# Kernel optimization log

Hardware: AMD Instinct MI355X
Metric: run time of the kernel (lower is better)

Reference implementation:

```python
import jax, jax.numpy as jnp
import numpy as np

B, T, D = 4096, 200, 64
N_USERS, N_ITEMS = 100000, 100000


def _linear_init(k, out_dim, in_dim):
    kw, kb = jax.random.split(k)
    lim = 1.0 / np.sqrt(in_dim)
    w = jax.random.uniform(kw, (out_dim, in_dim), minval=-lim, maxval=lim, dtype=jnp.float32)
    b = jax.random.uniform(kb, (out_dim,), minval=-lim, maxval=lim, dtype=jnp.float32)
    return w, b


def setup_inputs() -> dict:
    key = jax.random.key(0)
    ks = jax.random.split(key, 16)
    gru_w_ih, gru_b_ih = _linear_init(ks[0], 3 * D, D)   # torch GRU gate order: r, z, n
    gru_w_hh, gru_b_hh = _linear_init(ks[1], 3 * D, D)
    attn_w, attn_b = _linear_init(ks[2], D, D)
    wr_w, wr_b = _linear_init(ks[3], D, 2 * D)
    wz_w, wz_b = _linear_init(ks[4], D, 2 * D)
    wh_w, wh_b = _linear_init(ks[5], D, 2 * D)
    aux_w, aux_b = _linear_init(ks[6], 1, D)
    item_emb = jax.random.normal(ks[7], (N_ITEMS + 1, D), dtype=jnp.float32)
    user_bias = jax.random.normal(ks[8], (N_USERS, 1), dtype=jnp.float32) * 0.01
    item_bias = jax.random.normal(ks[9], (N_ITEMS, 1), dtype=jnp.float32) * 0.01
    u_idx = jax.random.randint(ks[10], (B,), 0, N_USERS)
    i_idx = jax.random.randint(ks[11], (B,), 0, N_ITEMS)
    seq = jax.random.randint(ks[12], (B, T), 0, N_ITEMS + 1)
    return dict(u_idx=u_idx, i_idx=i_idx, seq=seq,
                item_emb=item_emb, user_bias=user_bias, item_bias=item_bias,
                gru_w_ih=gru_w_ih, gru_b_ih=gru_b_ih, gru_w_hh=gru_w_hh, gru_b_hh=gru_b_hh,
                attn_w=attn_w, attn_b=attn_b,
                wr_w=wr_w, wr_b=wr_b, wz_w=wz_w, wz_b=wz_b, wh_w=wh_w, wh_b=wh_b,
                aux_w=aux_w, aux_b=aux_b)


def _gru(seq_emb, w_ih, b_ih, w_hh, b_hh):
    # seq_emb: [B, T, D]. Precompute input projections for all timesteps.
    x_proj = jnp.einsum('btd,gd->btg', seq_emb, w_ih) + b_ih  # [B, T, 3D]
    x_proj = jnp.transpose(x_proj, (1, 0, 2))                 # [T, B, 3D]
    h0 = jnp.zeros((seq_emb.shape[0], D), dtype=seq_emb.dtype)

    def step(h, xp):
        gh = h @ w_hh.T + b_hh
        xr, xz, xn = jnp.split(xp, 3, axis=-1)
        hr, hz, hn = jnp.split(gh, 3, axis=-1)
        r = jax.nn.sigmoid(xr + hr)
        z = jax.nn.sigmoid(xz + hz)
        n = jnp.tanh(xn + r * hn)
        h_new = (1.0 - z) * n + z * h
        return h_new, h_new

    _, hs = jax.lax.scan(step, h0, x_proj)
    return jnp.transpose(hs, (1, 0, 2))  # [B, T, D]


def _augru(seq_emb, attn_w_t, wr_w, wr_b, wz_w, wz_b, wh_w, wh_b):
    # Split each [D, 2D] weight into x-part and h-part (input was concat([x, h])).
    wr_x, wr_h = wr_w[:, :D], wr_w[:, D:]
    wz_x, wz_h = wz_w[:, :D], wz_w[:, D:]
    wh_x, wh_h = wh_w[:, :D], wh_w[:, D:]
    xr = jnp.einsum('btd,hd->bth', seq_emb, wr_x) + wr_b  # [B, T, D]
    xz = jnp.einsum('btd,hd->bth', seq_emb, wz_x) + wz_b
    xh = jnp.einsum('btd,hd->bth', seq_emb, wh_x) + wh_b
    h0 = jnp.zeros((seq_emb.shape[0], D), dtype=seq_emb.dtype)
    inputs = (jnp.transpose(xr, (1, 0, 2)), jnp.transpose(xz, (1, 0, 2)),
              jnp.transpose(xh, (1, 0, 2)), attn_w_t.T)  # [T,B,D]x3, [T,B]

    def step(h, inp):
        xr_t, xz_t, xh_t, a_t = inp
        r = jax.nn.sigmoid(xr_t + h @ wr_h.T)
        z = jax.nn.sigmoid(xz_t + h @ wz_h.T)
        h_hat = jnp.tanh(xh_t + (r * h) @ wh_h.T)
        z = a_t[:, None] * z
        h_new = (1.0 - z) * h + z * h_hat
        return h_new, None

    h_final, _ = jax.lax.scan(step, h0, inputs)
    return h_final  # [B, D]


def reference(u_idx, i_idx, seq, item_emb, user_bias, item_bias,
              gru_w_ih, gru_b_ih, gru_w_hh, gru_b_hh, attn_w, attn_b,
              wr_w, wr_b, wz_w, wz_b, wh_w, wh_b, aux_w, aux_b):
    fm1 = user_bias[u_idx] + item_bias[i_idx]          # [B, 1]
    target_emb = item_emb[i_idx]                       # [B, D]
    seq_emb = item_emb[seq]                            # [B, T, D]

    gru_out = _gru(seq_emb, gru_w_ih, gru_b_ih, gru_w_hh, gru_b_hh)  # [B, T, D]

    target_proj = target_emb @ attn_w.T + attn_b       # [B, D]
    attn_scores = jnp.einsum('btd,bd->bt', gru_out, target_proj)
    attn_weights = jax.nn.sigmoid(attn_scores)         # [B, T]

    attn_vec = _augru(seq_emb, attn_weights, wr_w, wr_b, wz_w, wz_b, wh_w, wh_b)  # [B, D]

    aux_logits = (gru_out[:, -1, :] @ aux_w.T + aux_b)[:, 0]  # [B]
    return (fm1, attn_vec, aux_logits)
```

## Files before the change

### kernel.cpp

```cpp
#include <hip/hip_runtime.h>

typedef __bf16 bf16x8 __attribute__((ext_vector_type(8)));
typedef float f32x4 __attribute__((ext_vector_type(4)));

#define T_LEN 200
#define NB 4096

__device__ __forceinline__ f32x4 mfma16(bf16x8 a, bf16x8 b, f32x4 c) {
    return __builtin_amdgcn_mfma_f32_16x16x32_bf16(a, b, c, 0, 0, 0);
}
__device__ __forceinline__ float sigf(float x) {
    return __builtin_amdgcn_rcpf(1.0f + __expf(-x));
}
__device__ __forceinline__ float tanh_fast(float x) {
    return 1.0f - 2.0f * __builtin_amdgcn_rcpf(__expf(2.0f * x) + 1.0f);
}

__device__ __forceinline__ unsigned packRNE2(float a, float b) {
    unsigned ha = (unsigned)__builtin_bit_cast(unsigned short, (__bf16)a);
    unsigned hb = (unsigned)__builtin_bit_cast(unsigned short, (__bf16)b);
    return ha | (hb << 16);
}
__device__ __forceinline__ void publish_hi(unsigned short* hp, float v) {
    __bf16 h = (__bf16)v;
    *hp = __builtin_bit_cast(unsigned short, h);
}

struct Frag { bf16x8 hi, lo; };
__device__ __forceinline__ Frag make_frag(f32x4 a, f32x4 b) {
    Frag f;
    #pragma unroll
    for (int j = 0; j < 4; j++) {
        float v = a[j]; __bf16 h = (__bf16)v;
        f.hi[j] = h; f.lo[j] = (__bf16)(v - (float)h);
    }
    #pragma unroll
    for (int j = 0; j < 4; j++) {
        float v = b[j]; __bf16 h = (__bf16)v;
        f.hi[4 + j] = h; f.lo[4 + j] = (__bf16)(v - (float)h);
    }
    return f;
}
__device__ __forceinline__ bf16x8 load_w(const float* p) {
    f32x4 a = *(const f32x4*)p, b = *(const f32x4*)(p + 4);
    bf16x8 w;
    #pragma unroll
    for (int j = 0; j < 4; j++) { w[j] = (__bf16)a[j]; w[4 + j] = (__bf16)b[j]; }
    return w;
}

__global__ __launch_bounds__(512, 2)
void dien_fused(const int* __restrict__ u_idx, const int* __restrict__ i_idx,
                const int* __restrict__ seq, const float* __restrict__ item_emb,
                const float* __restrict__ user_bias, const float* __restrict__ item_bias,
                const float* __restrict__ gw_ih, const float* __restrict__ gb_ih,
                const float* __restrict__ gw_hh, const float* __restrict__ gb_hh,
                const float* __restrict__ attn_w, const float* __restrict__ attn_b,
                const float* __restrict__ wr_w, const float* __restrict__ wr_b,
                const float* __restrict__ wz_w, const float* __restrict__ wz_b,
                const float* __restrict__ wh_w, const float* __restrict__ wh_b,
                const float* __restrict__ aux_w, const float* __restrict__ aux_b,
                float* __restrict__ out)
{
    __shared__ int sSeq[16][T_LEN];
    __shared__ __align__(16) float sTP[16][64];
    __shared__ __align__(16) unsigned short sHGhi[16][72];
    __shared__ __align__(16) unsigned short sHAhi[16][72];
    __shared__ __align__(16) unsigned short sRHhi[16][72];
    __shared__ __align__(16) unsigned short sXhi[16][72];
    __shared__ float sScore[2][16];
    __shared__ float sParts[16][4];

    const int tid  = threadIdx.x;
    const int wave = tid >> 6;
    const int lane = tid & 63;
    const int c    = lane & 15;
    const int q    = lane >> 4;
    const bool isG = (wave < 4);
    const int wg   = wave & 3;
    const int dglob = wg * 16 + c;
    const int row0 = blockIdx.x * 16;

    for (int i = tid; i < 16 * T_LEN; i += 512) {
        int b = i / T_LEN, t = i - b * T_LEN;
        sSeq[b][t] = seq[(row0 + b) * T_LEN + t];
    }

    if (tid < 16) {
        int b = row0 + tid;
        out[b] = user_bias[u_idx[b]] + item_bias[i_idx[b]];
    }

    if (tid < 256) {
        int b  = tid >> 4;
        int d0 = (tid & 15) * 4;
        const float* erow = item_emb + (long)i_idx[row0 + b] * 64;
        float e[64];
        #pragma unroll
        for (int k4 = 0; k4 < 16; k4++) {
            f32x4 v = *(const f32x4*)(erow + k4 * 4);
            #pragma unroll
            for (int j = 0; j < 4; j++) e[k4 * 4 + j] = v[j];
        }
        #pragma unroll
        for (int dd = 0; dd < 4; dd++) {
            int d = d0 + dd;
            const float* wrow = attn_w + d * 64;
            float s = attn_b[d];
            #pragma unroll
            for (int k4 = 0; k4 < 16; k4++) {
                f32x4 wv = *(const f32x4*)(wrow + k4 * 4);
                #pragma unroll
                for (int j = 0; j < 4; j++) s += e[k4 * 4 + j] * wv[j];
            }
            sTP[b][d] = s;
        }
    }

    for (int i = tid; i < 16 * 72; i += 512) sHAhi[0][i] = 0;
    const int xrow = wg * 4 + (lane >> 4);
    const int xch  = lane & 15;
    if (isG) {
        const float* p = item_emb + (long)seq[(row0 + xrow) * T_LEN + 0] * 64 + xch * 4;
        f32x4 v = *(const f32x4*)p;
        *(uint2*)&sXhi[xrow][xch * 4] =
            make_uint2(packRNE2(v[0], v[1]), packRNE2(v[2], v[3]));
    }
    __syncthreads();

    bf16x8 W[12];
    if (isG) {
        #pragma unroll
        for (int g = 0; g < 3; g++)
            #pragma unroll
            for (int s = 0; s < 2; s++) {
                W[g * 2 + s]     = load_w(gw_ih + (g * 64 + dglob) * 64 + s * 32 + q * 8);
                W[6 + g * 2 + s] = load_w(gw_hh + (g * 64 + dglob) * 64 + s * 32 + q * 8);
            }
    } else {
        #pragma unroll
        for (int s = 0; s < 2; s++) {
            const int fo = dglob * 128 + s * 32 + q * 8;
            W[0 + s]  = load_w(wr_w + fo);
            W[2 + s]  = load_w(wr_w + fo + 64);
            W[4 + s]  = load_w(wz_w + fo);
            W[6 + s]  = load_w(wz_w + fo + 64);
            W[8 + s]  = load_w(wh_w + fo);
            W[10 + s] = load_w(wh_w + fo + 64);
        }
    }

    float bA, bB, bC, bD;
    if (isG) {
        bA = gb_ih[dglob] + gb_hh[dglob];
        bB = gb_ih[64 + dglob] + gb_hh[64 + dglob];
        bC = gb_ih[128 + dglob];
        bD = gb_hh[128 + dglob];
    } else {
        bA = wr_b[dglob];
        bB = wz_b[dglob];
        bC = wh_b[dglob];
        bD = 0.0f;
    }
    const float auxwc = aux_w[dglob];

    Frag tpB0, tpB1;
    if (isG) {
        tpB0 = make_frag(*(const f32x4*)&sTP[c][q * 8], *(const f32x4*)&sTP[c][q * 8 + 4]);
        tpB1 = make_frag(*(const f32x4*)&sTP[c][32 + q * 8], *(const f32x4*)&sTP[c][32 + q * 8 + 4]);
    }

    float hst[4] = {0.f, 0.f, 0.f, 0.f};
    bf16x8 fr0, fr1;
    #pragma unroll
    for (int j = 0; j < 8; j++) { fr0[j] = (__bf16)0.f; fr1[j] = (__bf16)0.f; }
    f32x4 aAH = {0.f, 0.f, 0.f, 0.f};
    float z_c[4] = {0.f, 0.f, 0.f, 0.f};

    f32x4 xnxt = {0.f, 0.f, 0.f, 0.f};
    if (isG) {
        int t1 = (T_LEN > 1) ? 1 : 0;
        xnxt = *(const f32x4*)(item_emb + (long)sSeq[xrow][t1] * 64 + xch * 4);
    }

    for (int t = 0; t < T_LEN; t++) {
        f32x4 xg;
        f32x4 aAR, aAZ;

        bf16x8 x0 = *(const bf16x8*)&sXhi[c][q * 8];
        bf16x8 x1 = *(const bf16x8*)&sXhi[c][32 + q * 8];

        if (isG) {
            int tn = t + 2; if (tn > T_LEN - 1) tn = T_LEN - 1;
            xg = *(const f32x4*)(item_emb + (long)sSeq[xrow][tn] * 64 + xch * 4);

            f32x4 accR = {bA, bA, bA, bA};
            accR = mfma16(x0, W[0], accR); accR = mfma16(x1, W[1], accR);
            accR = mfma16(fr0, W[6], accR); accR = mfma16(fr1, W[7], accR);
            f32x4 accZ = {bB, bB, bB, bB};
            accZ = mfma16(x0, W[2], accZ); accZ = mfma16(x1, W[3], accZ);
            accZ = mfma16(fr0, W[8], accZ); accZ = mfma16(fr1, W[9], accZ);
            f32x4 accNX = {bC, bC, bC, bC};
            accNX = mfma16(x0, W[4], accNX); accNX = mfma16(x1, W[5], accNX);
            f32x4 accNH = {bD, bD, bD, bD};
            accNH = mfma16(fr0, W[10], accNH); accNH = mfma16(fr1, W[11], accNH);

            #pragma unroll
            for (int i = 0; i < 4; i++) {
                float r = sigf(accR[i]);
                float z = sigf(accZ[i]);
                float n = tanh_fast(accNX[i] + r * accNH[i]);
                float hn = n + z * (hst[i] - n);
                hst[i] = hn;
                publish_hi(&sHGhi[q * 4 + i][dglob], hn);
            }
        } else {
            if (t > 0) {
                bf16x8 rh0 = *(const bf16x8*)&sRHhi[c][q * 8];
                bf16x8 rh1 = *(const bf16x8*)&sRHhi[c][32 + q * 8];
                aAH = mfma16(rh0, W[10], aAH); aAH = mfma16(rh1, W[11], aAH);
                #pragma unroll
                for (int i = 0; i < 4; i++) {
                    int rr = q * 4 + i;
                    float a = sScore[(t - 1) & 1][rr];
                    float hh = tanh_fast(aAH[i]);
                    float zz = a * z_c[i];
                    float hv = hst[i] + zz * (hh - hst[i]);
                    hst[i] = hv;
                    publish_hi(&sHAhi[rr][dglob], hv);
                }
            }
            aAR = (f32x4){bA, bA, bA, bA};
            aAR = mfma16(x0, W[0], aAR); aAR = mfma16(x1, W[1], aAR);
            aAZ = (f32x4){bB, bB, bB, bB};
            aAZ = mfma16(x0, W[4], aAZ); aAZ = mfma16(x1, W[5], aAZ);
            aAH = (f32x4){bC, bC, bC, bC};
            aAH = mfma16(x0, W[8], aAH); aAH = mfma16(x1, W[9], aAH);
        }

        __syncthreads();

        if (isG) {
            fr0 = *(const bf16x8*)&sHGhi[c][q * 8];
            fr1 = *(const bf16x8*)&sHGhi[c][32 + q * 8];
            f32x4 sc = {0.f, 0.f, 0.f, 0.f};
            sc = mfma16(fr0, tpB0.hi, sc); sc = mfma16(fr0, tpB0.lo, sc);
            sc = mfma16(fr1, tpB1.hi, sc); sc = mfma16(fr1, tpB1.lo, sc);
            if (wg == 0 && (c >> 2) == q) {
                int i = c & 3;
                float d = (i == 0) ? sc[0] : (i == 1) ? sc[1] : (i == 2) ? sc[2] : sc[3];
                sScore[t & 1][c] = sigf(d);
            }
            *(uint2*)&sXhi[xrow][xch * 4] =
                make_uint2(packRNE2(xnxt[0], xnxt[1]), packRNE2(xnxt[2], xnxt[3]));
            xnxt = xg;
        } else {
            bf16x8 ha0 = *(const bf16x8*)&sHAhi[c][q * 8];
            bf16x8 ha1 = *(const bf16x8*)&sHAhi[c][32 + q * 8];
            aAR = mfma16(ha0, W[2], aAR); aAR = mfma16(ha1, W[3], aAR);
            aAZ = mfma16(ha0, W[6], aAZ); aAZ = mfma16(ha1, W[7], aAZ);
            #pragma unroll
            for (int i = 0; i < 4; i++) {
                float r = sigf(aAR[i]);
                z_c[i]  = sigf(aAZ[i]);
                float rh = r * hst[i];
                publish_hi(&sRHhi[q * 4 + i][dglob], rh);
            }
        }

        __syncthreads();
    }

    if (!isG) {
        bf16x8 rh0 = *(const bf16x8*)&sRHhi[c][q * 8];
        bf16x8 rh1 = *(const bf16x8*)&sRHhi[c][32 + q * 8];
        aAH = mfma16(rh0, W[10], aAH); aAH = mfma16(rh1, W[11], aAH);
        #pragma unroll
        for (int i = 0; i < 4; i++) {
            int rr = q * 4 + i;
            float a = sScore[(T_LEN - 1) & 1][rr];
            float hh = tanh_fast(aAH[i]);
            float zz = a * z_c[i];
            float hv = hst[i] + zz * (hh - hst[i]);
            out[NB + (row0 + rr) * 64 + dglob] = hv;
        }
    }

    if (isG) {
        float pa[4];
        #pragma unroll
        for (int i = 0; i < 4; i++) pa[i] = hst[i] * auxwc;
        #pragma unroll
        for (int m = 1; m < 16; m <<= 1) {
            #pragma unroll
            for (int i = 0; i < 4; i++) pa[i] += __shfl_xor(pa[i], m, 64);
        }
        if (c == 0) {
            #pragma unroll
            for (int i = 0; i < 4; i++) sParts[q * 4 + i][wg] = pa[i];
        }
    }
    __syncthreads();
    if (tid < 16) {
        out[NB + NB * 64 + row0 + tid] =
            sParts[tid][0] + sParts[tid][1] + sParts[tid][2] + sParts[tid][3] + aux_b[0];
    }
}

extern "C" void kernel_launch(void* const* d_in, const int* in_sizes, int n_in,
                              void* d_out, int out_size, void* d_ws, size_t ws_size,
                              hipStream_t stream) {
    dien_fused<<<dim3(256), dim3(512), 0, stream>>>(
        (const int*)d_in[0],
        (const int*)d_in[1],
        (const int*)d_in[2],
        (const float*)d_in[3],
        (const float*)d_in[4],
        (const float*)d_in[5],
        (const float*)d_in[6],
        (const float*)d_in[7],
        (const float*)d_in[8],
        (const float*)d_in[9],
        (const float*)d_in[10],
        (const float*)d_in[11],
        (const float*)d_in[12],
        (const float*)d_in[13],
        (const float*)d_in[14],
        (const float*)d_in[15],
        (const float*)d_in[16],
        (const float*)d_in[17],
        (const float*)d_in[18],
        (const float*)d_in[19],
        (float*)d_out);
}
```

Baseline: 263.6 us.

## Double-buffer input tile and precompute next-step input projections off the critical path

The shared input tile becomes double-buffered, and the input-side MFMA projections for step t+1 are computed in the second half of step t. At the start of each step only the recurrent hidden-state MFMAs stay on the dependency chain. This aims to shorten the serial per-timestep latency at the cost of extra accumulator registers and a second input buffer in shared memory.

Result: slower. 284.0 us (+7.7%).

```diff
diff --git a/kernel.cpp b/kernel.cpp
--- a/kernel.cpp
+++ b/kernel.cpp
@@ -15,7 +15,6 @@
 __device__ __forceinline__ float tanh_fast(float x) {
     return 1.0f - 2.0f * __builtin_amdgcn_rcpf(__expf(2.0f * x) + 1.0f);
 }
-
 __device__ __forceinline__ unsigned packRNE2(float a, float b) {
     unsigned ha = (unsigned)__builtin_bit_cast(unsigned short, (__bf16)a);
     unsigned hb = (unsigned)__builtin_bit_cast(unsigned short, (__bf16)b);
@@ -25,7 +24,6 @@
     __bf16 h = (__bf16)v;
     *hp = __builtin_bit_cast(unsigned short, h);
 }
-
 struct Frag { bf16x8 hi, lo; };
 __device__ __forceinline__ Frag make_frag(f32x4 a, f32x4 b) {
     Frag f;
@@ -67,7 +65,7 @@
     __shared__ __align__(16) unsigned short sHGhi[16][72];
     __shared__ __align__(16) unsigned short sHAhi[16][72];
     __shared__ __align__(16) unsigned short sRHhi[16][72];
-    __shared__ __align__(16) unsigned short sXhi[16][72];
+    __shared__ __align__(16) unsigned short sX[2][16][72];
     __shared__ float sScore[2][16];
     __shared__ float sParts[16][4];
 
@@ -118,12 +116,12 @@
     }
 
     for (int i = tid; i < 16 * 72; i += 512) sHAhi[0][i] = 0;
-    const int xrow = wg * 4 + (lane >> 4);
-    const int xch  = lane & 15;
+    const int xrow = wg * 4 + q;
+    const int xch  = c;
     if (isG) {
         const float* p = item_emb + (long)seq[(row0 + xrow) * T_LEN + 0] * 64 + xch * 4;
         f32x4 v = *(const f32x4*)p;
-        *(uint2*)&sXhi[xrow][xch * 4] =
+        *(uint2*)&sX[0][xrow][xch * 4] =
             make_uint2(packRNE2(v[0], v[1]), packRNE2(v[2], v[3]));
     }
     __syncthreads();
@@ -170,6 +168,23 @@
         tpB1 = make_frag(*(const f32x4*)&sTP[c][32 + q * 8], *(const f32x4*)&sTP[c][32 + q * 8 + 4]);
     }
 
+    f32x4 xpA, xpB, xpC;
+    {
+        bf16x8 x0 = *(const bf16x8*)&sX[0][c][q * 8];
+        bf16x8 x1 = *(const bf16x8*)&sX[0][c][32 + q * 8];
+        xpA = (f32x4){bA, bA, bA, bA};
+        xpA = mfma16(x0, W[0], xpA); xpA = mfma16(x1, W[1], xpA);
+        xpB = (f32x4){bB, bB, bB, bB};
+        xpC = (f32x4){bC, bC, bC, bC};
+        if (isG) {
+            xpB = mfma16(x0, W[2], xpB); xpB = mfma16(x1, W[3], xpB);
+            xpC = mfma16(x0, W[4], xpC); xpC = mfma16(x1, W[5], xpC);
+        } else {
+            xpB = mfma16(x0, W[4], xpB); xpB = mfma16(x1, W[5], xpB);
+            xpC = mfma16(x0, W[8], xpC); xpC = mfma16(x1, W[9], xpC);
+        }
+    }
+
     float hst[4] = {0.f, 0.f, 0.f, 0.f};
     bf16x8 fr0, fr1;
     #pragma unroll
@@ -178,30 +193,22 @@
     float z_c[4] = {0.f, 0.f, 0.f, 0.f};
 
     f32x4 xnxt = {0.f, 0.f, 0.f, 0.f};
-    if (isG) {
-        int t1 = (T_LEN > 1) ? 1 : 0;
-        xnxt = *(const f32x4*)(item_emb + (long)sSeq[xrow][t1] * 64 + xch * 4);
-    }
+    if (isG) xnxt = *(const f32x4*)(item_emb + (long)sSeq[xrow][1] * 64 + xch * 4);
 
     for (int t = 0; t < T_LEN; t++) {
         f32x4 xg;
         f32x4 aAR, aAZ;
 
-        bf16x8 x0 = *(const bf16x8*)&sXhi[c][q * 8];
-        bf16x8 x1 = *(const bf16x8*)&sXhi[c][32 + q * 8];
-
         if (isG) {
+            *(uint2*)&sX[(t + 1) & 1][xrow][xch * 4] =
+                make_uint2(packRNE2(xnxt[0], xnxt[1]), packRNE2(xnxt[2], xnxt[3]));
             int tn = t + 2; if (tn > T_LEN - 1) tn = T_LEN - 1;
             xg = *(const f32x4*)(item_emb + (long)sSeq[xrow][tn] * 64 + xch * 4);
 
-            f32x4 accR = {bA, bA, bA, bA};
-            accR = mfma16(x0, W[0], accR); accR = mfma16(x1, W[1], accR);
+            f32x4 accR = xpA;
             accR = mfma16(fr0, W[6], accR); accR = mfma16(fr1, W[7], accR);
-            f32x4 accZ = {bB, bB, bB, bB};
-            accZ = mfma16(x0, W[2], accZ); accZ = mfma16(x1, W[3], accZ);
+            f32x4 accZ = xpB;
             accZ = mfma16(fr0, W[8], accZ); accZ = mfma16(fr1, W[9], accZ);
-            f32x4 accNX = {bC, bC, bC, bC};
-            accNX = mfma16(x0, W[4], accNX); accNX = mfma16(x1, W[5], accNX);
             f32x4 accNH = {bD, bD, bD, bD};
             accNH = mfma16(fr0, W[10], accNH); accNH = mfma16(fr1, W[11], accNH);
 
@@ -209,7 +216,7 @@
             for (int i = 0; i < 4; i++) {
                 float r = sigf(accR[i]);
                 float z = sigf(accZ[i]);
-                float n = tanh_fast(accNX[i] + r * accNH[i]);
+                float n = tanh_fast(xpC[i] + r * accNH[i]);
                 float hn = n + z * (hst[i] - n);
                 hst[i] = hn;
                 publish_hi(&sHGhi[q * 4 + i][dglob], hn);
@@ -230,15 +237,15 @@
                     publish_hi(&sHAhi[rr][dglob], hv);
                 }
             }
-            aAR = (f32x4){bA, bA, bA, bA};
-            aAR = mfma16(x0, W[0], aAR); aAR = mfma16(x1, W[1], aAR);
-            aAZ = (f32x4){bB, bB, bB, bB};
-            aAZ = mfma16(x0, W[4], aAZ); aAZ = mfma16(x1, W[5], aAZ);
-            aAH = (f32x4){bC, bC, bC, bC};
-            aAH = mfma16(x0, W[8], aAH); aAH = mfma16(x1, W[9], aAH);
+            aAR = xpA;
+            aAZ = xpB;
+            aAH = xpC;
         }
 
         __syncthreads();
+
+        bf16x8 nx0 = *(const bf16x8*)&sX[(t + 1) & 1][c][q * 8];
+        bf16x8 nx1 = *(const bf16x8*)&sX[(t + 1) & 1][c][32 + q * 8];
 
         if (isG) {
             fr0 = *(const bf16x8*)&sHGhi[c][q * 8];
@@ -251,8 +258,12 @@
                 float d = (i == 0) ? sc[0] : (i == 1) ? sc[1] : (i == 2) ? sc[2] : sc[3];
                 sScore[t & 1][c] = sigf(d);
             }
-            *(uint2*)&sXhi[xrow][xch * 4] =
-                make_uint2(packRNE2(xnxt[0], xnxt[1]), packRNE2(xnxt[2], xnxt[3]));
+            xpA = (f32x4){bA, bA, bA, bA};
+            xpA = mfma16(nx0, W[0], xpA); xpA = mfma16(nx1, W[1], xpA);
+            xpB = (f32x4){bB, bB, bB, bB};
+            xpB = mfma16(nx0, W[2], xpB); xpB = mfma16(nx1, W[3], xpB);
+            xpC = (f32x4){bC, bC, bC, bC};
+            xpC = mfma16(nx0, W[4], xpC); xpC = mfma16(nx1, W[5], xpC);
             xnxt = xg;
         } else {
             bf16x8 ha0 = *(const bf16x8*)&sHAhi[c][q * 8];
@@ -266,6 +277,12 @@
                 float rh = r * hst[i];
                 publish_hi(&sRHhi[q * 4 + i][dglob], rh);
             }
+            xpA = (f32x4){bA, bA, bA, bA};
+            xpA = mfma16(nx0, W[0], xpA); xpA = mfma16(nx1, W[1], xpA);
+            xpB = (f32x4){bB, bB, bB, bB};
+            xpB = mfma16(nx0, W[4], xpB); xpB = mfma16(nx1, W[5], xpB);
+            xpC = (f32x4){bC, bC, bC, bC};
+            xpC = mfma16(nx0, W[8], xpC); xpC = mfma16(nx1, W[9], xpC);
         }
 
         __syncthreads();
```
